# Kernel tuning notes

Measured on AMD Instinct MI355X. Metric: run time of the kernel, lower is better.

## Reference

```python
import jax, jax.numpy as jnp
import numpy as np

B, S, D = 4, 1024, 1024
H, HD = 16, 64  # num_heads, head_dim; H*HD == D (qkv_features)
NEG_BIG = -1e10


def setup_inputs() -> dict:
    key = jax.random.key(0)
    ks = jax.random.split(key, 16)
    inp = {
        'inputs_q': jax.random.normal(ks[0], (B, S, D), jnp.float32),
        'inputs_kv': jax.random.normal(ks[1], (B, S, D), jnp.float32),
        'pos_emb_q': jax.random.normal(ks[2], (B, S, D), jnp.float32),
        'pos_emb_k': jax.random.normal(ks[3], (B, S, D), jnp.float32),
        'pos_emb_v': jax.random.normal(ks[4], (B, S, D), jnp.float32),
        'key_padding_mask': jnp.ones((B, S), jnp.float32),
    }
    scale = 1.0 / np.sqrt(D)
    inp['wq'] = jax.random.normal(ks[5], (D, H, HD), jnp.float32) * scale
    inp['bq'] = jnp.zeros((H, HD), jnp.float32)
    inp['wk'] = jax.random.normal(ks[6], (D, H, HD), jnp.float32) * scale
    inp['bk'] = jnp.zeros((H, HD), jnp.float32)
    inp['wv'] = jax.random.normal(ks[7], (D, H, HD), jnp.float32) * scale
    inp['bv'] = jnp.zeros((H, HD), jnp.float32)
    inp['wo'] = jax.random.normal(ks[8], (H, HD, D), jnp.float32) * scale
    inp['bo'] = jnp.zeros((D,), jnp.float32)
    return inp


def reference(inputs_q, inputs_kv, pos_emb_q, pos_emb_k, pos_emb_v,
              key_padding_mask, wq, bq, wk, bk, wv, bv, wo, bo):
    # Add positional embeddings before QKV projections (DETR style).
    q_in = inputs_q + pos_emb_q
    k_in = inputs_kv + pos_emb_k
    v_in = inputs_kv + pos_emb_v
    # DenseGeneral: [b,s,f] x [f,h,d] -> [b,s,h,d]
    q = jnp.einsum('bsf,fhd->bshd', q_in, wq) + bq
    k = jnp.einsum('bsf,fhd->bshd', k_in, wk) + bk
    v = jnp.einsum('bsf,fhd->bshd', v_in, wv) + bv
    # Additive key-padding bias, broadcast to [b,1,1,kv].
    bias = ((1.0 - key_padding_mask) * NEG_BIG)[:, None, None, :]
    q = q / jnp.sqrt(jnp.asarray(HD, q.dtype))
    attn = jnp.einsum('bqhd,bkhd->bhqk', q, k) + bias
    attn = jax.nn.softmax(attn, axis=-1)
    # (train=False: no dropout; identity capture layer is a no-op.)
    x = jnp.einsum('bhqk,bkhd->bqhd', attn, v)
    # Output projection over (heads, head_dim).
    out = jnp.einsum('bqhd,hdf->bqf', x, wo) + bo
    return out
```

## Files before the change

kernel.cpp:

```cpp
#include <hip/hip_runtime.h>
#include <hip/hip_bf16.h>
#include <stdint.h>

typedef __bf16 bf16_t;
typedef __bf16 bf16x8 __attribute__((ext_vector_type(8)));
typedef __bf16 bf16x4v __attribute__((ext_vector_type(4)));
typedef float  f32x4  __attribute__((ext_vector_type(4)));
typedef float  f32x16 __attribute__((ext_vector_type(16)));
typedef unsigned int u32;
typedef u32 u32x4 __attribute__((ext_vector_type(4)));

#define NEG_BIG (-1e10f)

__device__ __forceinline__ void load_lds16(const void* gsrc, void* ldst) {
  __builtin_amdgcn_global_load_lds(
      (__attribute__((address_space(1))) void*)(gsrc),
      (__attribute__((address_space(3))) void*)(ldst), 16, 0, 0);
}

__device__ __forceinline__ u32 cvt_pk_bf16(float lo, float hi) {
  u32 r;
  asm("v_cvt_pk_bf16_f32 %0, %1, %2" : "=v"(r) : "v"(lo), "v"(hi));
  return r;
}

__global__ __launch_bounds__(256) void k_prep_w(
    const float* __restrict__ iq, const float* __restrict__ ikv,
    const float* __restrict__ pq, const float* __restrict__ pk, const float* __restrict__ pv,
    const float* __restrict__ wq, const float* __restrict__ wk,
    const float* __restrict__ wv, const float* __restrict__ wo,
    bf16_t* __restrict__ Xq, bf16_t* __restrict__ Xk, bf16_t* __restrict__ Xv,
    bf16_t* __restrict__ Wt, bf16_t* __restrict__ Wot)
{
  __shared__ float t[64][65];
  if (blockIdx.x < 4096) {
    int i = blockIdx.x * 256 + threadIdx.x;
    float4 a = ((const float4*)iq)[i], b = ((const float4*)ikv)[i];
    float4 eq = ((const float4*)pq)[i], ek = ((const float4*)pk)[i], ev = ((const float4*)pv)[i];
    bf16x4v q, k, v;
    q[0] = (bf16_t)(a.x + eq.x); q[1] = (bf16_t)(a.y + eq.y);
    q[2] = (bf16_t)(a.z + eq.z); q[3] = (bf16_t)(a.w + eq.w);
    k[0] = (bf16_t)(b.x + ek.x); k[1] = (bf16_t)(b.y + ek.y);
    k[2] = (bf16_t)(b.z + ek.z); k[3] = (bf16_t)(b.w + ek.w);
    v[0] = (bf16_t)(b.x + ev.x); v[1] = (bf16_t)(b.y + ev.y);
    v[2] = (bf16_t)(b.z + ev.z); v[3] = (bf16_t)(b.w + ev.w);
    *(bf16x4v*)&Xq[(size_t)i*4] = q;
    *(bf16x4v*)&Xk[(size_t)i*4] = k;
    *(bf16x4v*)&Xv[(size_t)i*4] = v;
  } else {
    int bid = blockIdx.x - 4096;
    int z = bid >> 8, rem = bid & 255;
    const float* src = z==0 ? wq : z==1 ? wk : z==2 ? wv : wo;
    bf16_t*      dst = z < 3 ? (Wt + (size_t)z*(1u<<20)) : Wot;
    int n0 = (rem & 15) << 6, k0 = (rem >> 4) << 6;
    int c = threadIdx.x & 63, rb = threadIdx.x >> 6;
    #pragma unroll
    for (int i = 0; i < 16; ++i) {
      int r = i*4 + rb;
      t[r][c] = src[(size_t)(k0 + r)*1024 + n0 + c];
    }
    __syncthreads();
    #pragma unroll
    for (int i = 0; i < 16; ++i) {
      int r = i*4 + rb;
      dst[(size_t)(n0 + r)*1024 + k0 + c] = (bf16_t)t[c][r];
    }
  }
}

__global__ __launch_bounds__(256, 2) void k_gemm_qkv(
    const bf16_t* __restrict__ Xq, const bf16_t* __restrict__ Xk, const bf16_t* __restrict__ Xv,
    const bf16_t* __restrict__ Wt,
    const float* __restrict__ bq, const float* __restrict__ bk, const float* __restrict__ bv,
    bf16_t* __restrict__ Qo, bf16_t* __restrict__ Ko, bf16_t* __restrict__ Vt)
{
  const int L = blockIdx.x;
  const int w = (L & 7) * 96 + (L >> 3);
  const int bn = w >> 5, by = w & 31;
  const int z = bn >> 3;
  const bf16_t* A = z==0 ? Xq : z==1 ? Xk : Xv;
  const float* bias = z==0 ? bq : z==1 ? bk : bv;

  __shared__ bf16_t As[2][128*64];
  __shared__ bf16_t Bs[2][128*64];

  const int tid = threadIdx.x, lane = tid & 63, wid = tid >> 6;
  const int wm = wid >> 1, wn = wid & 1;
  const int bm0 = by * 128;
  const int bn0g = bn * 128;
  const int g = lane >> 4, c = lane & 15;
  const int sr = lane >> 3, sch = lane & 7;

  f32x4 acc[4][4] = {};

  #define STAGE(bufi, kt_)                                                       \
    { _Pragma("unroll")                                                          \
      for (int i = 0; i < 4; ++i) {                                              \
        int r  = wid*32 + i*8 + sr;                                              \
        int ca = sch ^ (r & 7);                                                  \
        load_lds16(A  + (size_t)(bm0  + r)*1024 + (size_t)(kt_)*64 + ca*8,       \
                   &As[bufi][(wid*32 + i*8)*64]);                                \
        load_lds16(Wt + (size_t)(bn0g + r)*1024 + (size_t)(kt_)*64 + ca*8,       \
                   &Bs[bufi][(wid*32 + i*8)*64]);                                \
      } }

  STAGE(0, 0);
  STAGE(1, 1);
  asm volatile("s_waitcnt vmcnt(8)" ::: "memory");
  __builtin_amdgcn_sched_barrier(0);
  __builtin_amdgcn_s_barrier();
  __builtin_amdgcn_sched_barrier(0);

  for (int kt = 0; kt < 16; ++kt) {
    const int buf = kt & 1;

    __builtin_amdgcn_s_setprio(1);
    #pragma unroll
    for (int kk = 0; kk < 2; ++kk) {
      bf16x8 af[4], bfr[4];
      #pragma unroll
      for (int m = 0; m < 4; ++m) {
        int row = wm*64 + m*16 + c;
        int ch  = (kk*4 + g) ^ (row & 7);
        af[m] = *(const bf16x8*)&As[buf][row*64 + ch*8];
      }
      #pragma unroll
      for (int n = 0; n < 4; ++n) {
        int row = wn*64 + n*16 + c;
        int ch  = (kk*4 + g) ^ (row & 7);
        bfr[n] = *(const bf16x8*)&Bs[buf][row*64 + ch*8];
      }
      #pragma unroll
      for (int m = 0; m < 4; ++m)
        #pragma unroll
        for (int n = 0; n < 4; ++n)
          acc[m][n] = __builtin_amdgcn_mfma_f32_16x16x32_bf16(af[m], bfr[n], acc[m][n], 0, 0, 0);
    }
    __builtin_amdgcn_s_setprio(0);

    if (kt < 15) {
      __builtin_amdgcn_sched_barrier(0);
      __builtin_amdgcn_s_barrier();
      __builtin_amdgcn_sched_barrier(0);
      if (kt < 14) {
        STAGE(buf, kt + 2);
        asm volatile("s_waitcnt vmcnt(8)" ::: "memory");
      } else {
        asm volatile("s_waitcnt vmcnt(0)" ::: "memory");
      }
      __builtin_amdgcn_sched_barrier(0);
      __builtin_amdgcn_s_barrier();
      __builtin_amdgcn_sched_barrier(0);
    }
  }
  #undef STAGE

  if (z < 2) {
    bf16_t* C = z==0 ? Qo : Ko;
    const float scale = z==0 ? 0.125f : 1.0f;
    #pragma unroll
    for (int n = 0; n < 4; ++n) {
      int col = (bn0g & 1023) + wn*64 + n*16 + c;
      float bn_ = bias[col];
      #pragma unroll
      for (int m = 0; m < 4; ++m) {
        int row0 = bm0 + wm*64 + m*16 + g*4;
        #pragma unroll
        for (int r = 0; r < 4; ++r)
          C[(size_t)(row0 + r)*1024 + col] = (bf16_t)((acc[m][n][r] + bn_) * scale);
      }
    }
  } else {
    #pragma unroll
    for (int n = 0; n < 4; ++n) {
      int colz = (bn0g & 1023) + wn*64 + n*16 + c;
      float bn_ = bias[colz];
      int h = colz >> 6, hd = colz & 63;
      #pragma unroll
      for (int m = 0; m < 4; ++m) {
        int row0 = bm0 + wm*64 + m*16 + g*4;
        int b = row0 >> 10, s0 = row0 & 1023;
        bf16x4v v4;
        #pragma unroll
        for (int r = 0; r < 4; ++r) v4[r] = (bf16_t)(acc[m][n][r] + bn_);
        *(bf16x4v*)&Vt[(size_t)((b*16 + h)*64 + hd)*1024 + s0] = v4;
      }
    }
  }
}

__global__ __launch_bounds__(256, 2) void k_attn2(
    const bf16_t* __restrict__ Qm, const bf16_t* __restrict__ Km,
    const bf16_t* __restrict__ Vt, const float* __restrict__ mask,
    bf16_t* __restrict__ X2)
{
  __shared__ bf16_t Ks[2][64*64];
  __shared__ bf16_t Vs[2][64*64];
  __shared__ float  bias_lds[1024];
  __shared__ float  l_lds[4][32];

  const int qt = blockIdx.x, h = blockIdx.y, b = blockIdx.z;
  const int tid = threadIdx.x, lane = tid & 63, wid = tid >> 6;
  const int lq = lane & 31;
  const int hi = lane >> 5;

  {
    float4 m4 = *(const float4*)&mask[b*1024 + tid*4];
    float4 b4;
    b4.x = (1.0f - m4.x) * NEG_BIG;
    b4.y = (1.0f - m4.y) * NEG_BIG;
    b4.z = (1.0f - m4.z) * NEG_BIG;
    b4.w = (1.0f - m4.w) * NEG_BIG;
    *(float4*)&bias_lds[tid*4] = b4;
  }

  const int q0w = qt*128 + wid*32;
  bf16x8 qf[4];
  #pragma unroll
  for (int kb = 0; kb < 4; ++kb)
    qf[kb] = *(const bf16x8*)&Qm[(size_t)(b*1024 + q0w + lq)*1024 + h*64 + kb*16 + hi*8];

  f32x16 oacc[2] = {};
  float mrow = -1e30f, lsum = 0.f;

  const int sr8 = (lane >> 3);
  const int sc8 = lane & 7;
  #define STAGE(bufi, kv0)                                                        \
    {                                                                             \
      _Pragma("unroll")                                                           \
      for (int cc = 0; cc < 2; ++cc) {                                            \
        int r  = cc*32 + wid*8 + sr8;                                             \
        int ca = sc8 ^ (r & 7);                                                   \
        load_lds16(Km + (size_t)(b*1024 + (kv0) + r)*1024 + h*64 + ca*8,          \
                   &Ks[bufi][(cc*32 + wid*8)*64]);                                \
        load_lds16(Vt + (size_t)((b*16 + h)*64 + r)*1024 + (kv0) + ca*8,          \
                   &Vs[bufi][(cc*32 + wid*8)*64]);                                \
      }                                                                           \
    }

  STAGE(0, 0);
  __syncthreads();

  for (int kt = 0; kt < 16; ++kt) {
    const int buf = kt & 1;
    if (kt < 15) STAGE(buf ^ 1, (kt + 1) * 64);

    f32x16 s[2];
    #pragma unroll
    for (int blk = 0; blk < 2; ++blk) {
      f32x16 acc = {};
      #pragma unroll
      for (int kb = 0; kb < 4; ++kb) {
        int row = blk*32 + lq;
        int ch  = (kb*2 + hi) ^ (row & 7);
        bf16x8 kf = *(const bf16x8*)&Ks[buf][row*64 + ch*8];
        acc = __builtin_amdgcn_mfma_f32_32x32x16_bf16(kf, qf[kb], acc, 0, 0, 0);
      }
      s[blk] = acc;
    }

    #pragma unroll
    for (int blk = 0; blk < 2; ++blk)
      #pragma unroll
      for (int g2 = 0; g2 < 4; ++g2) {
        float4 b4 = *(const float4*)&bias_lds[kt*64 + blk*32 + g2*8 + hi*4];
        s[blk][g2*4+0] += b4.x;
        s[blk][g2*4+1] += b4.y;
        s[blk][g2*4+2] += b4.z;
        s[blk][g2*4+3] += b4.w;
      }

    float pmax = s[0][0];
    #pragma unroll
    for (int blk = 0; blk < 2; ++blk)
      #pragma unroll
      for (int r = 0; r < 16; ++r) pmax = fmaxf(pmax, s[blk][r]);
    pmax = fmaxf(pmax, __shfl_xor(pmax, 32, 64));

    if (!__all(pmax - mrow <= 8.0f)) {
      float mnew = fmaxf(mrow, pmax);
      float sc = __expf(mrow - mnew);
      lsum *= sc;
      #pragma unroll
      for (int nb = 0; nb < 2; ++nb)
        #pragma unroll
        for (int i = 0; i < 16; ++i) oacc[nb][i] *= sc;
      mrow = mnew;
    }

    float rs = 0.f;
    #pragma unroll
    for (int blk = 0; blk < 2; ++blk)
      #pragma unroll
      for (int r = 0; r < 16; ++r) {
        float p = __expf(s[blk][r] - mrow);
        s[blk][r] = p;
        rs += p;
      }
    lsum += rs + __shfl_xor(rs, 32, 64);

    u32 paw[4][4];
    #pragma unroll
    for (int blk = 0; blk < 2; ++blk)
      #pragma unroll
      for (int half = 0; half < 2; ++half) {
        int base = half * 8;
        #pragma unroll
        for (int w2 = 0; w2 < 2; ++w2) {
          u32 x = cvt_pk_bf16(s[blk][base + 2*w2],     s[blk][base + 2*w2 + 1]);
          u32 y = cvt_pk_bf16(s[blk][base + 4 + 2*w2], s[blk][base + 4 + 2*w2 + 1]);
          asm("v_permlane32_swap_b32 %0, %1" : "+v"(x), "+v"(y));
          paw[blk*2 + half][w2]     = x;
          paw[blk*2 + half][w2 + 2] = y;
        }
      }

    #pragma unroll
    for (int ks = 0; ks < 4; ++ks) {
      u32x4 t = { paw[ks][0], paw[ks][1], paw[ks][2], paw[ks][3] };
      bf16x8 pa = __builtin_bit_cast(bf16x8, t);
      #pragma unroll
      for (int nb = 0; nb < 2; ++nb) {
        int row = nb*32 + lq;
        int ch  = (ks*2 + hi) ^ (row & 7);
        bf16x8 vf = *(const bf16x8*)&Vs[buf][row*64 + ch*8];
        oacc[nb] = __builtin_amdgcn_mfma_f32_32x32x16_bf16(pa, vf, oacc[nb], 0, 0, 0);
      }
    }
    __syncthreads();
  }

  l_lds[wid][lq] = lsum;
  __syncthreads();
  #pragma unroll
  for (int g2 = 0; g2 < 4; ++g2)
    #pragma unroll
    for (int j = 0; j < 4; ++j) {
      int reg  = g2*4 + j;
      int qrow = j + 8*g2 + 4*hi;
      float inv = 1.0f / l_lds[wid][qrow];
      #pragma unroll
      for (int nb = 0; nb < 2; ++nb)
        X2[(size_t)(b*1024 + q0w + qrow)*1024 + h*64 + nb*32 + lq] =
            (bf16_t)(oacc[nb][reg] * inv);
    }
  #undef STAGE
}

__global__ __launch_bounds__(256, 2) void k_gemm_out(
    const bf16_t* __restrict__ A, const bf16_t* __restrict__ Bt,
    const float* __restrict__ bo, float* __restrict__ C)
{
  const int L = blockIdx.x;
  const int w = (L & 7) * 32 + (L >> 3);
  const int bn = w >> 5, by = w & 31;

  __shared__ bf16_t As[2][128*64];
  __shared__ bf16_t Bs[2][128*64];

  const int tid = threadIdx.x, lane = tid & 63, wid = tid >> 6;
  const int wm = wid >> 1, wn = wid & 1;
  const int bm0 = by * 128, bn0 = bn * 128;
  const int g = lane >> 4, c = lane & 15;
  const int sr = lane >> 3, sch = lane & 7;

  f32x4 acc[4][4] = {};

  #define STAGEO(bufi, kt_)                                                      \
    { _Pragma("unroll")                                                          \
      for (int i = 0; i < 4; ++i) {                                              \
        int r  = wid*32 + i*8 + sr;                                              \
        int ca = sch ^ (r & 7);                                                  \
        load_lds16(A  + (size_t)(bm0 + r)*1024 + (size_t)(kt_)*64 + ca*8,        \
                   &As[bufi][(wid*32 + i*8)*64]);                                \
        load_lds16(Bt + (size_t)(bn0 + r)*1024 + (size_t)(kt_)*64 + ca*8,        \
                   &Bs[bufi][(wid*32 + i*8)*64]);                                \
      } }

  STAGEO(0, 0);
  STAGEO(1, 1);
  asm volatile("s_waitcnt vmcnt(8)" ::: "memory");
  __builtin_amdgcn_sched_barrier(0);
  __builtin_amdgcn_s_barrier();
  __builtin_amdgcn_sched_barrier(0);

  for (int kt = 0; kt < 16; ++kt) {
    const int buf = kt & 1;

    __builtin_amdgcn_s_setprio(1);
    #pragma unroll
    for (int kk = 0; kk < 2; ++kk) {
      bf16x8 af[4], bfr[4];
      #pragma unroll
      for (int m = 0; m < 4; ++m) {
        int row = wm*64 + m*16 + c;
        int ch  = (kk*4 + g) ^ (row & 7);
        af[m] = *(const bf16x8*)&As[buf][row*64 + ch*8];
      }
      #pragma unroll
      for (int n = 0; n < 4; ++n) {
        int row = wn*64 + n*16 + c;
        int ch  = (kk*4 + g) ^ (row & 7);
        bfr[n] = *(const bf16x8*)&Bs[buf][row*64 + ch*8];
      }
      #pragma unroll
      for (int m = 0; m < 4; ++m)
        #pragma unroll
        for (int n = 0; n < 4; ++n)
          acc[m][n] = __builtin_amdgcn_mfma_f32_16x16x32_bf16(af[m], bfr[n], acc[m][n], 0, 0, 0);
    }
    __builtin_amdgcn_s_setprio(0);

    if (kt < 15) {
      __builtin_amdgcn_sched_barrier(0);
      __builtin_amdgcn_s_barrier();
      __builtin_amdgcn_sched_barrier(0);
      if (kt < 14) {
        STAGEO(buf, kt + 2);
        asm volatile("s_waitcnt vmcnt(8)" ::: "memory");
      } else {
        asm volatile("s_waitcnt vmcnt(0)" ::: "memory");
      }
      __builtin_amdgcn_sched_barrier(0);
      __builtin_amdgcn_s_barrier();
      __builtin_amdgcn_sched_barrier(0);
    }
  }
  #undef STAGEO

  #pragma unroll
  for (int n = 0; n < 4; ++n) {
    int col = bn0 + wn*64 + n*16 + c;
    float bn_ = bo[col];
    #pragma unroll
    for (int m = 0; m < 4; ++m) {
      int row0 = bm0 + wm*64 + m*16 + g*4;
      #pragma unroll
      for (int r = 0; r < 4; ++r)
        C[(size_t)(row0 + r)*1024 + col] = acc[m][n][r] + bn_;
    }
  }
}

extern "C" void kernel_launch(void* const* d_in, const int* in_sizes, int n_in,
                              void* d_out, int out_size, void* d_ws, size_t ws_size,
                              hipStream_t stream) {
  const float* iq   = (const float*)d_in[0];
  const float* ikv  = (const float*)d_in[1];
  const float* pq   = (const float*)d_in[2];
  const float* pk   = (const float*)d_in[3];
  const float* pv   = (const float*)d_in[4];
  const float* mask = (const float*)d_in[5];
  const float* wq   = (const float*)d_in[6];
  const float* bq   = (const float*)d_in[7];
  const float* wk   = (const float*)d_in[8];
  const float* bk   = (const float*)d_in[9];
  const float* wv   = (const float*)d_in[10];
  const float* bv   = (const float*)d_in[11];
  const float* wo   = (const float*)d_in[12];
  const float* bo   = (const float*)d_in[13];
  float* out = (float*)d_out;

  char* ws = (char*)d_ws;
  bf16_t* Xq  = (bf16_t*)(ws + (size_t)( 0u<<20));
  bf16_t* Xk  = (bf16_t*)(ws + (size_t)( 8u<<20));
  bf16_t* Xv  = (bf16_t*)(ws + (size_t)(16u<<20));
  bf16_t* Wt  = (bf16_t*)(ws + (size_t)(24u<<20));
  bf16_t* Wot = (bf16_t*)(ws + (size_t)(30u<<20));
  bf16_t* Q   = (bf16_t*)(ws + (size_t)(32u<<20));
  bf16_t* K   = (bf16_t*)(ws + (size_t)(40u<<20));
  bf16_t* Vt  = (bf16_t*)(ws + (size_t)(56u<<20));
  bf16_t* X2  = (bf16_t*)(ws + (size_t)(64u<<20));

  k_prep_w<<<5120, 256, 0, stream>>>(iq, ikv, pq, pk, pv, wq, wk, wv, wo,
                                     Xq, Xk, Xv, Wt, Wot);
  k_gemm_qkv<<<768, 256, 0, stream>>>(Xq, Xk, Xv, Wt, bq, bk, bv, Q, K, Vt);
  k_attn2<<<dim3(8,16,4), 256, 0, stream>>>(Q, K, Vt, mask, X2);
  k_gemm_out<<<256, 256, 0, stream>>>(X2, Wot, bo, out);
}
```

Before: 120.1 us.

## Replace double-buffered LDS pipeline with single-buffer GEMMs at higher occupancy

Both the QKV and output GEMM kernels drop their double-buffered LDS prefetch pipeline, along with the explicit vmcnt waits and setprio, and move to a single 32 KB LDS buffer with a load, sync, compute, sync loop per k-tile. Launch bounds rise from 2 to 3 blocks per CU so that more resident blocks can hide memory latency in place of in-block prefetch. The block-index decomposition is also reordered so that column tiles vary fastest. The trade-off is losing overlap of global loads with MFMA work inside each block and adding more barriers.

```diff
diff --git a/kernel.cpp b/kernel.cpp
--- a/kernel.cpp
+++ b/kernel.cpp
@@ -68,7 +68,7 @@
   }
 }
 
-__global__ __launch_bounds__(256, 2) void k_gemm_qkv(
+__global__ __launch_bounds__(256, 3) void k_gemm_qkv(
     const bf16_t* __restrict__ Xq, const bf16_t* __restrict__ Xk, const bf16_t* __restrict__ Xv,
     const bf16_t* __restrict__ Wt,
     const float* __restrict__ bq, const float* __restrict__ bk, const float* __restrict__ bv,
@@ -76,13 +76,14 @@
 {
   const int L = blockIdx.x;
   const int w = (L & 7) * 96 + (L >> 3);
-  const int bn = w >> 5, by = w & 31;
-  const int z = bn >> 3;
-  const bf16_t* A = z==0 ? Xq : z==1 ? Xk : Xv;
-  const float* bias = z==0 ? bq : z==1 ? bk : bv;
-
-  __shared__ bf16_t As[2][128*64];
-  __shared__ bf16_t Bs[2][128*64];
+  const int bx = w & 7, by = (w >> 3) & 31, bz = w >> 8;
+  const int bn = bz * 8 + bx;
+
+  const bf16_t* A = bz==0 ? Xq : bz==1 ? Xk : Xv;
+  const float* bias = bz==0 ? bq : bz==1 ? bk : bv;
+
+  __shared__ bf16_t As[128*64];
+  __shared__ bf16_t Bs[128*64];
 
   const int tid = threadIdx.x, lane = tid & 63, wid = tid >> 6;
   const int wm = wid >> 1, wn = wid & 1;
@@ -93,28 +94,20 @@
 
   f32x4 acc[4][4] = {};
 
-  #define STAGE(bufi, kt_)                                                       \
+  #define STAGE(kt_)                                                             \
     { _Pragma("unroll")                                                          \
       for (int i = 0; i < 4; ++i) {                                              \
         int r  = wid*32 + i*8 + sr;                                              \
         int ca = sch ^ (r & 7);                                                  \
         load_lds16(A  + (size_t)(bm0  + r)*1024 + (size_t)(kt_)*64 + ca*8,       \
-                   &As[bufi][(wid*32 + i*8)*64]);                                \
+                   &As[(wid*32 + i*8)*64]);                                      \
         load_lds16(Wt + (size_t)(bn0g + r)*1024 + (size_t)(kt_)*64 + ca*8,       \
-                   &Bs[bufi][(wid*32 + i*8)*64]);                                \
+                   &Bs[(wid*32 + i*8)*64]);                                      \
       } }
 
-  STAGE(0, 0);
-  STAGE(1, 1);
-  asm volatile("s_waitcnt vmcnt(8)" ::: "memory");
-  __builtin_amdgcn_sched_barrier(0);
-  __builtin_amdgcn_s_barrier();
-  __builtin_amdgcn_sched_barrier(0);
-
   for (int kt = 0; kt < 16; ++kt) {
-    const int buf = kt & 1;
-
-    __builtin_amdgcn_s_setprio(1);
+    STAGE(kt);
+    __syncthreads();
     #pragma unroll
     for (int kk = 0; kk < 2; ++kk) {
       bf16x8 af[4], bfr[4];
@@ -122,13 +115,13 @@
       for (int m = 0; m < 4; ++m) {
         int row = wm*64 + m*16 + c;
         int ch  = (kk*4 + g) ^ (row & 7);
-        af[m] = *(const bf16x8*)&As[buf][row*64 + ch*8];
+        af[m] = *(const bf16x8*)&As[row*64 + ch*8];
       }
       #pragma unroll
       for (int n = 0; n < 4; ++n) {
         int row = wn*64 + n*16 + c;
         int ch  = (kk*4 + g) ^ (row & 7);
-        bfr[n] = *(const bf16x8*)&Bs[buf][row*64 + ch*8];
+        bfr[n] = *(const bf16x8*)&Bs[row*64 + ch*8];
       }
       #pragma unroll
       for (int m = 0; m < 4; ++m)
@@ -136,28 +129,13 @@
         for (int n = 0; n < 4; ++n)
           acc[m][n] = __builtin_amdgcn_mfma_f32_16x16x32_bf16(af[m], bfr[n], acc[m][n], 0, 0, 0);
     }
-    __builtin_amdgcn_s_setprio(0);
-
-    if (kt < 15) {
-      __builtin_amdgcn_sched_barrier(0);
-      __builtin_amdgcn_s_barrier();
-      __builtin_amdgcn_sched_barrier(0);
-      if (kt < 14) {
-        STAGE(buf, kt + 2);
-        asm volatile("s_waitcnt vmcnt(8)" ::: "memory");
-      } else {
-        asm volatile("s_waitcnt vmcnt(0)" ::: "memory");
-      }
-      __builtin_amdgcn_sched_barrier(0);
-      __builtin_amdgcn_s_barrier();
-      __builtin_amdgcn_sched_barrier(0);
-    }
+    __syncthreads();
   }
   #undef STAGE
 
-  if (z < 2) {
-    bf16_t* C = z==0 ? Qo : Ko;
-    const float scale = z==0 ? 0.125f : 1.0f;
+  if (bz < 2) {
+    bf16_t* C = bz==0 ? Qo : Ko;
+    const float scale = bz==0 ? 0.125f : 1.0f;
     #pragma unroll
     for (int n = 0; n < 4; ++n) {
       int col = (bn0g & 1023) + wn*64 + n*16 + c;
@@ -347,47 +325,39 @@
   #undef STAGE
 }
 
-__global__ __launch_bounds__(256, 2) void k_gemm_out(
+__global__ __launch_bounds__(256, 3) void k_gemm_out(
     const bf16_t* __restrict__ A, const bf16_t* __restrict__ Bt,
     const float* __restrict__ bo, float* __restrict__ C)
 {
   const int L = blockIdx.x;
   const int w = (L & 7) * 32 + (L >> 3);
-  const int bn = w >> 5, by = w & 31;
-
-  __shared__ bf16_t As[2][128*64];
-  __shared__ bf16_t Bs[2][128*64];
+  const int bx = w & 7, by = w >> 3;
+
+  __shared__ bf16_t As[128*64];
+  __shared__ bf16_t Bs[128*64];
 
   const int tid = threadIdx.x, lane = tid & 63, wid = tid >> 6;
   const int wm = wid >> 1, wn = wid & 1;
-  const int bm0 = by * 128, bn0 = bn * 128;
+  const int bm0 = by * 128, bn0 = bx * 128;
   const int g = lane >> 4, c = lane & 15;
   const int sr = lane >> 3, sch = lane & 7;
 
   f32x4 acc[4][4] = {};
 
-  #define STAGEO(bufi, kt_)                                                      \
+  #define STAGEO(kt_)                                                            \
     { _Pragma("unroll")                                                          \
       for (int i = 0; i < 4; ++i) {                                              \
         int r  = wid*32 + i*8 + sr;                                              \
         int ca = sch ^ (r & 7);                                                  \
         load_lds16(A  + (size_t)(bm0 + r)*1024 + (size_t)(kt_)*64 + ca*8,        \
-                   &As[bufi][(wid*32 + i*8)*64]);                                \
+                   &As[(wid*32 + i*8)*64]);                                      \
         load_lds16(Bt + (size_t)(bn0 + r)*1024 + (size_t)(kt_)*64 + ca*8,        \
-                   &Bs[bufi][(wid*32 + i*8)*64]);                                \
+                   &Bs[(wid*32 + i*8)*64]);                                      \
       } }
 
-  STAGEO(0, 0);
-  STAGEO(1, 1);
-  asm volatile("s_waitcnt vmcnt(8)" ::: "memory");
-  __builtin_amdgcn_sched_barrier(0);
-  __builtin_amdgcn_s_barrier();
-  __builtin_amdgcn_sched_barrier(0);
-
   for (int kt = 0; kt < 16; ++kt) {
-    const int buf = kt & 1;
-
-    __builtin_amdgcn_s_setprio(1);
+    STAGEO(kt);
+    __syncthreads();
     #pragma unroll
     for (int kk = 0; kk < 2; ++kk) {
       bf16x8 af[4], bfr[4];
@@ -395,13 +365,13 @@
       for (int m = 0; m < 4; ++m) {
         int row = wm*64 + m*16 + c;
         int ch  = (kk*4 + g) ^ (row & 7);
-        af[m] = *(const bf16x8*)&As[buf][row*64 + ch*8];
+        af[m] = *(const bf16x8*)&As[row*64 + ch*8];
       }
       #pragma unroll
       for (int n = 0; n < 4; ++n) {
         int row = wn*64 + n*16 + c;
         int ch  = (kk*4 + g) ^ (row & 7);
-        bfr[n] = *(const bf16x8*)&Bs[buf][row*64 + ch*8];
+        bfr[n] = *(const bf16x8*)&Bs[row*64 + ch*8];
       }
       #pragma unroll
       for (int m = 0; m < 4; ++m)
@@ -409,22 +379,7 @@
         for (int n = 0; n < 4; ++n)
           acc[m][n] = __builtin_amdgcn_mfma_f32_16x16x32_bf16(af[m], bfr[n], acc[m][n], 0, 0, 0);
     }
-    __builtin_amdgcn_s_setprio(0);
-
-    if (kt < 15) {
-      __builtin_amdgcn_sched_barrier(0);
-      __builtin_amdgcn_s_barrier();
-      __builtin_amdgcn_sched_barrier(0);
-      if (kt < 14) {
-        STAGEO(buf, kt + 2);
-        asm volatile("s_waitcnt vmcnt(8)" ::: "memory");
-      } else {
-        asm volatile("s_waitcnt vmcnt(0)" ::: "memory");
-      }
-      __builtin_amdgcn_sched_barrier(0);
-      __builtin_amdgcn_s_barrier();
-      __builtin_amdgcn_sched_barrier(0);
-    }
+    __syncthreads();
   }
   #undef STAGEO
 
```

After: 112.1 us. 6.7% less time.
